# Performance work log

Measured on AMD Instinct MI355X. Metric: run time of the kernel, lower is better.

The kernel has to match this reference:

```python
import jax, jax.numpy as jnp
import numpy as np
from jax import lax

K = 3  # kernel_size

def _conv1d(inp, w, b, padding):
    # inp: [B, Cin, W], w: [Cout, Cin, K]
    y = lax.conv_general_dilated(inp, w, (1,), padding,
                                 dimension_numbers=('NCH', 'OIH', 'NCH'))
    return y + b[None, :, None]


def setup_inputs() -> dict:
    key = jax.random.key(0)
    ks = jax.random.split(key, 10)
    B, C, H, W = 8, 3, 512, 2048
    s = 0.1
    return {
        'x':  jax.random.normal(ks[0], (B, C, H, W), dtype=jnp.float32),
        'w1': jax.random.normal(ks[1], (5, 3, K),  dtype=jnp.float32) * s,
        'b1': jax.random.normal(ks[2], (5,),       dtype=jnp.float32) * s,
        'w2': jax.random.normal(ks[3], (10, 5, K), dtype=jnp.float32) * s,
        'b2': jax.random.normal(ks[4], (10,),      dtype=jnp.float32) * s,
        'wl': jax.random.normal(ks[5], (10, 12, K), dtype=jnp.float32) * s,
        'bl': jax.random.normal(ks[6], (10,),       dtype=jnp.float32) * s,
        'wo': jax.random.normal(ks[7], (1, 10),    dtype=jnp.float32) * s,  # 1x1 conv2d weight
        'bo': jax.random.normal(ks[8], (1,),       dtype=jnp.float32) * s,
    }


def reference(x, w1, b1, w2, b2, wl, bl, wo, bo):
    # x: [B, 3, num_steps, W]
    # Step 0: conv_first on stack([x[:,0,-1], x[:,1,0], x[:,2,0]])
    first_in = jnp.stack([x[:, 0, -1, :], x[:, 1, 0, :], x[:, 2, 0, :]], axis=1)  # [B,3,W]
    h = jax.nn.relu(_conv1d(first_in, w1, b1, 'VALID'))          # [B,5,W-2]
    h = jax.nn.relu(_conv1d(h, w2, b2, [(1, 1)]))                # [B,10,W-2] ('same')
    row0 = jnp.pad(h, ((0, 0), (0, 0), (1, 1)))                  # write into [:,:,0,1:-1]

    # Recurrence over steps 1..num_steps-1 (strict data dependence -> lax.scan)
    def step(prev, xi):
        # prev: [B,10,W], xi: [B,2,W]
        inp = jnp.concatenate([prev, xi], axis=1)                # [B,12,W]
        y = jax.nn.relu(_conv1d(inp, wl, bl, 'VALID'))           # [B,10,W-2]
        row = jnp.pad(y, ((0, 0), (0, 0), (1, 1)))               # [B,10,W]
        return row, row

    xs = jnp.moveaxis(x[:, 1:3, 1:, :], 2, 0)                    # [num_steps-1, B, 2, W]
    _, rows = lax.scan(step, row0, xs)                           # [num_steps-1, B, 10, W]

    pred = jnp.concatenate([row0[None], rows], axis=0)           # [num_steps, B, 10, W]
    pred = jnp.moveaxis(pred, 0, 2)                              # [B, 10, num_steps, W]

    # conv_to_result: 1x1 Conv2d, 10 -> 1 channels
    out = jnp.einsum('bchw,oc->bohw', pred, wo) + bo[None, :, None, None]
    return out
```

## Files before the change

kernel.cpp:

```cpp
#include <hip/hip_runtime.h>
#include <cstdint>

#define W 2048
#define H 512
#define K 32
#define NW 8
#define NSLOT 1058
#define ABASE 0
#define BBASE (NSLOT*4)
#define BUFD  10248
#define FLOFF (2*BUFD)

typedef __fp16 h2    __attribute__((ext_vector_type(2)));
typedef __fp16 f16x8 __attribute__((ext_vector_type(8)));
typedef float  f32x16 __attribute__((ext_vector_type(16)));

static __device__ __forceinline__ h2 as_h2(uint32_t u){ union{uint32_t u; h2 h;} x; x.u=u; return x.h; }
static __device__ __forceinline__ uint32_t as_u32(h2 h){ union{uint32_t u; h2 h;} x; x.h=h; return x.u; }

__global__ __launch_bounds__(512, 1) void recurrent_kernel(
    const float* __restrict__ x,
    const float* __restrict__ w1, const float* __restrict__ b1,
    const float* __restrict__ w2, const float* __restrict__ b2,
    const float* __restrict__ wl, const float* __restrict__ bl,
    const float* __restrict__ wo, const float* __restrict__ bo,
    float* __restrict__ out, uint32_t* __restrict__ ws)
{
    extern __shared__ uint32_t lds[];
    const int tid  = threadIdx.x;
    const int b    = blockIdx.x & 7;
    const int hfl  = blockIdx.x >> 3;
    const int lane = tid & 63;
    const int wvL  = tid >> 6;
    const int m    = lane & 31;
    const int hh   = lane >> 5;

    const int cbase = hfl ? 991 : -1;
    const int EW    = hfl ? 0 : 7;
    const bool isEW = (wvL == EW);
    const int nti   = isEW ? 5 : 4;
    const int hti   = hfl ? 0 : 4;
    const int sti   = hfl ? 1 : 3;
    const int obase = (isEW && hfl) ? 1 : 0;

    for (int i = tid; i < 2*BUFD + NW; i += 512) lds[i] = 0;

    f16x8 afrag[3];
    #pragma unroll
    for (int tap = 0; tap < 3; ++tap)
        #pragma unroll
        for (int j = 0; j < 8; ++j) {
            int k = 8*hh + j;
            float v = (m < 10 && k < 12) ? wl[(m*12 + k)*3 + tap] : 0.f;
            afrag[tap][j] = (__fp16)v;
        }
    h2 wop0, wop1, wop2;
    if (hh == 0) {
        wop0 = __builtin_amdgcn_cvt_pkrtz(wo[0], wo[1]);
        wop1 = __builtin_amdgcn_cvt_pkrtz(wo[2], wo[3]);
        wop2 = __builtin_amdgcn_cvt_pkrtz(wo[8], wo[9]);
    } else {
        wop0 = __builtin_amdgcn_cvt_pkrtz(wo[4], wo[5]);
        wop1 = __builtin_amdgcn_cvt_pkrtz(wo[6], wo[7]);
        wop2 = __builtin_amdgcn_cvt_pkrtz(0.f, 0.f);
    }
    f32x16 bias16;
    #pragma unroll
    for (int r = 0; r < 16; ++r) {
        int ch = (r & 3) + 8*(r >> 2) + 4*hh;
        bias16[r] = (r < 8 && ch < 10) ? bl[ch] : 0.f;
    }
    const float bov = bo[0];
    const int bpaddr = (lane ^ 32) << 2;
    const h2 hz = {(__fp16)0.f, (__fp16)0.f};

    const float* x1b = x + (((size_t)b*3 + 1)*H)*W;
    const float* x2b = x + (((size_t)b*3 + 2)*H)*W;
    float* outb = out + (size_t)b*H*W;

    int rdi_[5], aw_[5], bw_[5], col_[5];
    bool wok[5];
    #pragma unroll
    for (int ti = 0; ti < 5; ++ti) {
        int gt = (hfl == 0) ? (ti == 4 ? 32 : 4*wvL + ti)
                            : (wvL == 0 ? ti : 4*wvL + 1 + ti);
        int sb = 32*gt + m;
        rdi_[ti] = (hh ? BBASE : ABASE) + 4*sb;
        aw_[ti]  = ABASE + 4*(sb + 1) + 2*hh;
        bw_[ti]  = BBASE + 4*(sb + 1);
        col_[ti] = 32*gt + m + (hfl ? 992 : 0);
        wok[ti]  = (col_[ti] != 0) && (col_[ti] != W-1);
    }
    uint32_t* fl = lds + FLOFF;
    const int na = (wvL == 0)    ? wvL : wvL - 1;
    const int nb = (wvL == NW-1) ? wvL : wvL + 1;

    uint32_t* rec_m = ws + (b*2 + hfl)*512;
    uint32_t* rec_o = ws + (b*2 + (1 - hfl))*512;

    const int xbase = (hfl == 0) ? (128*wvL + 1) : (wvL == 0 ? 1 : 128*wvL + 33);
    const int xsl1 = xbase + lane;
    const int xsl2 = xbase + 64 + lane;
    const bool xe3 = isEW && (hh == 0);
    const int xsl3 = xbase + 128 + m;

    __syncthreads();

    for (int idx = tid; idx < NSLOT; idx += 512) {
        const int p = idx + cbase;
        float fi[3][5];
        #pragma unroll
        for (int l = 0; l < 5; ++l) {
            int v = p - 2 + l;
            bool ok = (v >= 0) && (v < W);
            fi[0][l] = ok ? x[(((size_t)b*3 + 0)*H + (H-1))*W + v] : 0.f;
            fi[1][l] = ok ? x1b[v] : 0.f;
            fi[2][l] = ok ? x2b[v] : 0.f;
        }
        float h1v[5][3];
        #pragma unroll
        for (int c = 0; c < 5; ++c)
            #pragma unroll
            for (int i3 = 0; i3 < 3; ++i3) {
                int u = p - 2 + i3;
                float a = b1[c];
                #pragma unroll
                for (int j = 0; j < 3; ++j)
                    #pragma unroll
                    for (int k = 0; k < 3; ++k)
                        a += w1[(c*3 + j)*3 + k] * fi[j][i3 + k];
                h1v[c][i3] = (u >= 0 && u <= W-3) ? fmaxf(a, 0.f) : 0.f;
            }
        const bool valid = (p >= 1) && (p <= W-2);
        float h2c[10];
        #pragma unroll
        for (int c2 = 0; c2 < 10; ++c2) {
            float a = b2[c2];
            #pragma unroll
            for (int c = 0; c < 5; ++c)
                #pragma unroll
                for (int k = 0; k < 3; ++k)
                    a += w2[(c2*5 + c)*3 + k] * h1v[c][k];
            h2c[c2] = valid ? fmaxf(a, 0.f) : 0.f;
        }
        uint4 wr;
        wr.x = as_u32(__builtin_amdgcn_cvt_pkrtz(h2c[0], h2c[1]));
        wr.y = as_u32(__builtin_amdgcn_cvt_pkrtz(h2c[2], h2c[3]));
        wr.z = as_u32(__builtin_amdgcn_cvt_pkrtz(h2c[4], h2c[5]));
        wr.w = as_u32(__builtin_amdgcn_cvt_pkrtz(h2c[6], h2c[7]));
        *(uint4*)(lds + ABASE + 4*idx) = wr;
        lds[BBASE + 4*idx] = as_u32(__builtin_amdgcn_cvt_pkrtz(h2c[8], h2c[9]));
        bool okp = (p >= 0) && (p < W);
        lds[BBASE + 4*idx + 1] = okp
            ? as_u32(__builtin_amdgcn_cvt_pkrtz(x1b[W + p], x2b[W + p])) : 0u;
        if (p >= hfl*1024 && p < hfl*1024 + 1024) {
            float s = bov;
            #pragma unroll
            for (int c = 0; c < 10; ++c) s += wo[c]*h2c[c];
            outb[p] = s;
        }
    }
    __syncthreads();

    #pragma unroll 1
    for (int t = 1; t < H; ++t) {
        const uint32_t* rb = lds + ((t - 1) & 1)*BUFD;
        uint32_t*       wb = lds + (t & 1)*BUFD;
        const bool sync = ((t & (K-1)) == 0);

        float xa1, xa2, xb1, xb2, xc1 = 0.f, xc2 = 0.f;
        const bool pf = (t + 1 < H);
        if (pf) {
            const float* r1 = x1b + (size_t)(t + 1)*W + cbase;
            const float* r2 = x2b + (size_t)(t + 1)*W + cbase;
            xa1 = r1[xsl1];  xa2 = r2[xsl1];
            xb1 = r1[xsl2];  xb2 = r2[xsl2];
            if (xe3) { xc1 = r1[xsl3]; xc2 = r2[xsl3]; }
        }

        if (t >= 2) {
            const uint32_t need = (uint32_t)(t - 1);
            while (__hip_atomic_load(&fl[na], __ATOMIC_ACQUIRE, __HIP_MEMORY_SCOPE_WORKGROUP) < need ||
                   __hip_atomic_load(&fl[nb], __ATOMIC_ACQUIRE, __HIP_MEMORY_SCOPE_WORKGROUP) < need)
                __builtin_amdgcn_s_sleep(1);
        }

        uint4 bu[5][3];
        #pragma unroll
        for (int ti = 0; ti < 5; ++ti)
            if (ti < nti)
                #pragma unroll
                for (int tap = 0; tap < 3; ++tap)
                    bu[ti][tap] = *(const uint4*)(rb + rdi_[ti] + 4*tap);

        uint32_t stash[5][3];
        float pv[5];
        #pragma unroll
        for (int ti = 0; ti < 5; ++ti) {
            if (ti >= nti) continue;
            union { uint4 u; f16x8 v; } c0, c1, c2;
            c0.u = bu[ti][0]; c1.u = bu[ti][1]; c2.u = bu[ti][2];
            f32x16 acc = __builtin_amdgcn_mfma_f32_32x32x16_f16(afrag[0], c0.v, bias16, 0, 0, 0);
            acc = __builtin_amdgcn_mfma_f32_32x32x16_f16(afrag[1], c1.v, acc, 0, 0, 0);
            acc = __builtin_amdgcn_mfma_f32_32x32x16_f16(afrag[2], c2.v, acc, 0, 0, 0);
            h2 p0 = __builtin_elementwise_max(__builtin_amdgcn_cvt_pkrtz(acc[0], acc[1]), hz);
            h2 p1 = __builtin_elementwise_max(__builtin_amdgcn_cvt_pkrtz(acc[2], acc[3]), hz);
            h2 p2 = __builtin_elementwise_max(__builtin_amdgcn_cvt_pkrtz(acc[4], acc[5]), hz);
            stash[ti][0] = as_u32(p0); stash[ti][1] = as_u32(p1); stash[ti][2] = as_u32(p2);
            float pc = __builtin_amdgcn_fdot2(wop2, p2,
                       __builtin_amdgcn_fdot2(wop1, p1,
                       __builtin_amdgcn_fdot2(wop0, p0, 0.f, false), false), false);
            int pi = __builtin_amdgcn_ds_bpermute(bpaddr, __builtin_bit_cast(int, pc));
            pv[ti] = pc + __builtin_bit_cast(float, pi);
        }

        if (sync && isEW) {
            uint32_t* rec = rec_m + (((t >> 5) & 1) ? 256 : 0);
            if (hh == 0) {
                __hip_atomic_store(rec + 32 +   0 + m, stash[sti][0], __ATOMIC_RELAXED, __HIP_MEMORY_SCOPE_AGENT);
                __hip_atomic_store(rec + 32 +  32 + m, stash[sti][1], __ATOMIC_RELAXED, __HIP_MEMORY_SCOPE_AGENT);
                __hip_atomic_store(rec + 32 + 128 + m, stash[sti][2], __ATOMIC_RELAXED, __HIP_MEMORY_SCOPE_AGENT);
            } else {
                __hip_atomic_store(rec + 32 +  64 + m, stash[sti][0], __ATOMIC_RELAXED, __HIP_MEMORY_SCOPE_AGENT);
                __hip_atomic_store(rec + 32 +  96 + m, stash[sti][1], __ATOMIC_RELAXED, __HIP_MEMORY_SCOPE_AGENT);
            }
            if (lane == 0)
                __hip_atomic_store(rec, (uint32_t)t, __ATOMIC_RELEASE, __HIP_MEMORY_SCOPE_AGENT);
        }

        #pragma unroll
        for (int ti = 0; ti < 5; ++ti) {
            if (ti >= nti) continue;
            bool skip_halo = sync && isEW && (ti == hti);
            if (wok[ti] && !skip_halo) {
                uint32_t* rp = wb + aw_[ti];
                uint2 wr; wr.x = stash[ti][0]; wr.y = stash[ti][1];
                *(uint2*)rp = wr;
                if (hh == 0) wb[bw_[ti]] = stash[ti][2];
            }
        }
        if (pf) {
            wb[BBASE + 4*xsl1 + 1] = as_u32(__builtin_amdgcn_cvt_pkrtz(xa1, xa2));
            wb[BBASE + 4*xsl2 + 1] = as_u32(__builtin_amdgcn_cvt_pkrtz(xb1, xb2));
            if (xe3) wb[BBASE + 4*xsl3 + 1] = as_u32(__builtin_amdgcn_cvt_pkrtz(xc1, xc2));
        }

        if (lane == 0)
            __hip_atomic_store(&fl[wvL], (uint32_t)t, __ATOMIC_RELEASE, __HIP_MEMORY_SCOPE_WORKGROUP);

        if (sync && isEW) {
            uint32_t* rec = rec_o + (((t >> 5) & 1) ? 256 : 0);
            while (__hip_atomic_load(rec, __ATOMIC_ACQUIRE, __HIP_MEMORY_SCOPE_AGENT) < (uint32_t)t)
                __builtin_amdgcn_s_sleep(2);
            const int rslot = (hfl ? 1 : 1025) + m;
            if (hh == 0) {
                uint32_t d0 = __hip_atomic_load(rec + 32 +   0 + m, __ATOMIC_RELAXED, __HIP_MEMORY_SCOPE_AGENT);
                uint32_t d1 = __hip_atomic_load(rec + 32 +  32 + m, __ATOMIC_RELAXED, __HIP_MEMORY_SCOPE_AGENT);
                uint32_t d2 = __hip_atomic_load(rec + 32 + 128 + m, __ATOMIC_RELAXED, __HIP_MEMORY_SCOPE_AGENT);
                uint2 wr; wr.x = d0; wr.y = d1;
                *(uint2*)(wb + ABASE + 4*rslot) = wr;
                wb[BBASE + 4*rslot] = d2;
            } else {
                uint32_t d0 = __hip_atomic_load(rec + 32 +  64 + m, __ATOMIC_RELAXED, __HIP_MEMORY_SCOPE_AGENT);
                uint32_t d1 = __hip_atomic_load(rec + 32 +  96 + m, __ATOMIC_RELAXED, __HIP_MEMORY_SCOPE_AGENT);
                uint2 wr; wr.x = d0; wr.y = d1;
                *(uint2*)(wb + ABASE + 4*rslot + 2) = wr;
            }
        }

        #pragma unroll
        for (int i = 0; i < 2; ++i) {
            const int oti = obase + 2*hh + i;
            const int c = col_[oti];
            float val = (c == 0 || c == W-1) ? bov : pv[oti] + bov;
            outb[(size_t)t*W + c] = val;
        }
    }
}

extern "C" void kernel_launch(void* const* d_in, const int* in_sizes, int n_in,
                              void* d_out, int out_size, void* d_ws, size_t ws_size,
                              hipStream_t stream)
{
    const float* x  = (const float*)d_in[0];
    const float* w1 = (const float*)d_in[1];
    const float* b1 = (const float*)d_in[2];
    const float* w2 = (const float*)d_in[3];
    const float* b2 = (const float*)d_in[4];
    const float* wl = (const float*)d_in[5];
    const float* bl = (const float*)d_in[6];
    const float* wo = (const float*)d_in[7];
    const float* bo = (const float*)d_in[8];
    float* out = (float*)d_out;

    hipMemsetAsync(d_ws, 0, 8*2*512*sizeof(uint32_t), stream);

    const int shbytes = (2*BUFD + NW) * sizeof(uint32_t);
    hipFuncSetAttribute((const void*)recurrent_kernel,
                        hipFuncAttributeMaxDynamicSharedMemorySize, shbytes);
    recurrent_kernel<<<16, 512, shbytes, stream>>>(x, w1, b1, w2, b2, wl, bl, wo, bo,
                                                   out, (uint32_t*)d_ws);
}
```

Baseline: 895.3 us.

## Compute interior tiles before waiting on neighbor-wave flags; move output store earlier

Each wave's tiles are split into interior tiles, which do not depend on neighbouring waves' fresh writes, and edge tiles, which do. Interior tiles are loaded, computed and written before the spin-wait on neighbour flags, so the MFMA work overlaps the inter-wave synchronisation. Edge tiles are handled after the wait. The global output store is also moved ahead of the cross-block exchange wait so it is not held up by that wait. This relies on the gating table correctly marking which tiles read halo data from other waves; a mislabelled tile would read stale data.

```diff
diff --git a/kernel.cpp b/kernel.cpp
--- a/kernel.cpp
+++ b/kernel.cpp
@@ -79,7 +79,7 @@
     float* outb = out + (size_t)b*H*W;
 
     int rdi_[5], aw_[5], bw_[5], col_[5];
-    bool wok[5];
+    bool wok[5], gated_[5];
     #pragma unroll
     for (int ti = 0; ti < 5; ++ti) {
         int gt = (hfl == 0) ? (ti == 4 ? 32 : 4*wvL + ti)
@@ -90,6 +90,9 @@
         bw_[ti]  = BBASE + 4*(sb + 1);
         col_[ti] = 32*gt + m + (hfl ? 992 : 0);
         wok[ti]  = (col_[ti] != 0) && (col_[ti] != W-1);
+        if (!isEW)          gated_[ti] = (ti == 0) || (ti == 3);
+        else if (hfl == 0)  gated_[ti] = (ti == 0);
+        else                gated_[ti] = (ti == 4);
     }
     uint32_t* fl = lds + FLOFF;
     const int na = (wvL == 0)    ? wvL : wvL - 1;
@@ -178,26 +181,11 @@
             if (xe3) { xc1 = r1[xsl3]; xc2 = r2[xsl3]; }
         }
 
-        if (t >= 2) {
-            const uint32_t need = (uint32_t)(t - 1);
-            while (__hip_atomic_load(&fl[na], __ATOMIC_ACQUIRE, __HIP_MEMORY_SCOPE_WORKGROUP) < need ||
-                   __hip_atomic_load(&fl[nb], __ATOMIC_ACQUIRE, __HIP_MEMORY_SCOPE_WORKGROUP) < need)
-                __builtin_amdgcn_s_sleep(1);
-        }
-
         uint4 bu[5][3];
-        #pragma unroll
-        for (int ti = 0; ti < 5; ++ti)
-            if (ti < nti)
-                #pragma unroll
-                for (int tap = 0; tap < 3; ++tap)
-                    bu[ti][tap] = *(const uint4*)(rb + rdi_[ti] + 4*tap);
-
         uint32_t stash[5][3];
         float pv[5];
-        #pragma unroll
-        for (int ti = 0; ti < 5; ++ti) {
-            if (ti >= nti) continue;
+
+        auto tilecomp = [&](int ti) {
             union { uint4 u; f16x8 v; } c0, c1, c2;
             c0.u = bu[ti][0]; c1.u = bu[ti][1]; c2.u = bu[ti][2];
             f32x16 acc = __builtin_amdgcn_mfma_f32_32x32x16_f16(afrag[0], c0.v, bias16, 0, 0, 0);
@@ -212,7 +200,29 @@
                        __builtin_amdgcn_fdot2(wop0, p0, 0.f, false), false), false);
             int pi = __builtin_amdgcn_ds_bpermute(bpaddr, __builtin_bit_cast(int, pc));
             pv[ti] = pc + __builtin_bit_cast(float, pi);
-        }
+        };
+        auto tilewrite = [&](int ti) {
+            bool skip_halo = sync && isEW && (ti == hti);
+            if (wok[ti] && !skip_halo) {
+                uint32_t* rp = wb + aw_[ti];
+                uint2 wr; wr.x = stash[ti][0]; wr.y = stash[ti][1];
+                *(uint2*)rp = wr;
+                if (hh == 0) wb[bw_[ti]] = stash[ti][2];
+            }
+        };
+
+        #pragma unroll
+        for (int ti = 0; ti < 5; ++ti)
+            if (ti < nti && !gated_[ti])
+                #pragma unroll
+                for (int tap = 0; tap < 3; ++tap)
+                    bu[ti][tap] = *(const uint4*)(rb + rdi_[ti] + 4*tap);
+        #pragma unroll
+        for (int ti = 0; ti < 5; ++ti)
+            if (ti < nti && !gated_[ti]) tilecomp(ti);
+        #pragma unroll
+        for (int ti = 0; ti < 5; ++ti)
+            if (ti < nti && !gated_[ti]) tilewrite(ti);
 
         if (sync && isEW) {
             uint32_t* rec = rec_m + (((t >> 5) & 1) ? 256 : 0);
@@ -228,17 +238,26 @@
                 __hip_atomic_store(rec, (uint32_t)t, __ATOMIC_RELEASE, __HIP_MEMORY_SCOPE_AGENT);
         }
 
-        #pragma unroll
-        for (int ti = 0; ti < 5; ++ti) {
-            if (ti >= nti) continue;
-            bool skip_halo = sync && isEW && (ti == hti);
-            if (wok[ti] && !skip_halo) {
-                uint32_t* rp = wb + aw_[ti];
-                uint2 wr; wr.x = stash[ti][0]; wr.y = stash[ti][1];
-                *(uint2*)rp = wr;
-                if (hh == 0) wb[bw_[ti]] = stash[ti][2];
-            }
-        }
+        if (t >= 2) {
+            const uint32_t need = (uint32_t)(t - 1);
+            while (__hip_atomic_load(&fl[na], __ATOMIC_ACQUIRE, __HIP_MEMORY_SCOPE_WORKGROUP) < need ||
+                   __hip_atomic_load(&fl[nb], __ATOMIC_ACQUIRE, __HIP_MEMORY_SCOPE_WORKGROUP) < need)
+                __builtin_amdgcn_s_sleep(1);
+        }
+
+        #pragma unroll
+        for (int ti = 0; ti < 5; ++ti)
+            if (ti < nti && gated_[ti])
+                #pragma unroll
+                for (int tap = 0; tap < 3; ++tap)
+                    bu[ti][tap] = *(const uint4*)(rb + rdi_[ti] + 4*tap);
+        #pragma unroll
+        for (int ti = 0; ti < 5; ++ti)
+            if (ti < nti && gated_[ti]) tilecomp(ti);
+        #pragma unroll
+        for (int ti = 0; ti < 5; ++ti)
+            if (ti < nti && gated_[ti]) tilewrite(ti);
+
         if (pf) {
             wb[BBASE + 4*xsl1 + 1] = as_u32(__builtin_amdgcn_cvt_pkrtz(xa1, xa2));
             wb[BBASE + 4*xsl2 + 1] = as_u32(__builtin_amdgcn_cvt_pkrtz(xb1, xb2));
@@ -247,6 +266,14 @@
 
         if (lane == 0)
             __hip_atomic_store(&fl[wvL], (uint32_t)t, __ATOMIC_RELEASE, __HIP_MEMORY_SCOPE_WORKGROUP);
+
+        #pragma unroll
+        for (int i = 0; i < 2; ++i) {
+            const int oti = obase + 2*hh + i;
+            const int c = col_[oti];
+            float val = (c == 0 || c == W-1) ? bov : pv[oti] + bov;
+            outb[(size_t)t*W + c] = val;
+        }
 
         if (sync && isEW) {
             uint32_t* rec = rec_o + (((t >> 5) & 1) ? 256 : 0);
@@ -267,14 +294,6 @@
                 *(uint2*)(wb + ABASE + 4*rslot + 2) = wr;
             }
         }
-
-        #pragma unroll
-        for (int i = 0; i < 2; ++i) {
-            const int oti = obase + 2*hh + i;
-            const int c = col_[oti];
-            float val = (c == 0 || c == W-1) ? bov : pv[oti] + bov;
-            outb[(size_t)t*W + c] = val;
-        }
     }
 }
 
```

Result: slower. 1.047 ms (+16.9%).
